# Optimization experiments

Measured on AMD Instinct MI355X. Metric: run time of the kernel, lower is better.

## Reference

```python
import jax, jax.numpy as jnp
import numpy as np

B, S, D = 2, 2048, 2048
H, KV, HD = 16, 4, 128          # n_heads, n_kv_heads, head_dim = d_model // n_heads
R = H // KV                      # n_rep (GQA group size)
THETA = 500000.0


def _rotate_half(x):
    x1, x2 = jnp.split(x, 2, axis=-1)
    return jnp.concatenate([-x2, x1], axis=-1)


def _rope_cos_sin(position_ids):
    # inv_freq over even dims, outer with positions, duplicated (LLaMA-style)
    inv_freq = 1.0 / (THETA ** (jnp.arange(0, HD, 2, dtype=jnp.float32) / HD))
    freqs = position_ids.astype(jnp.float32)[..., None] * inv_freq  # (B, S, HD/2)
    emb = jnp.concatenate([freqs, freqs], axis=-1)                  # (B, S, HD)
    return jnp.cos(emb)[:, None], jnp.sin(emb)[:, None]             # (B, 1, S, HD)


def setup_inputs() -> dict:
    key = jax.random.key(0)
    ks = jax.random.split(key, 5)
    x = jax.random.normal(ks[0], (B, S, D), dtype=jnp.float32)
    wq = jax.random.normal(ks[1], (D, H * HD), dtype=jnp.float32) * (D ** -0.5)
    wk = jax.random.normal(ks[2], (D, KV * HD), dtype=jnp.float32) * (D ** -0.5)
    wv = jax.random.normal(ks[3], (D, KV * HD), dtype=jnp.float32) * (D ** -0.5)
    wo = jax.random.normal(ks[4], (H * HD, D), dtype=jnp.float32) * (D ** -0.5)
    causal = jnp.tril(jnp.ones((S, S), dtype=bool))
    attn_mask = jnp.where(causal, 0.0, -1e9).astype(jnp.float32)[None, None]  # (1,1,S,S)
    position_ids = jnp.tile(jnp.arange(S, dtype=jnp.int32)[None, :], (B, 1))
    return {"x": x, "wq": wq, "wk": wk, "wv": wv, "wo": wo,
            "attn_mask": attn_mask, "position_ids": position_ids}


def reference(x, wq, wk, wv, wo, attn_mask, position_ids):
    b, s, _ = x.shape
    # projections (bias-free Linear) + head split, (B, heads, S, HD)
    q = (x @ wq).reshape(b, s, H, HD).transpose(0, 2, 1, 3)
    k = (x @ wk).reshape(b, s, KV, HD).transpose(0, 2, 1, 3)
    v = (x @ wv).reshape(b, s, KV, HD).transpose(0, 2, 1, 3)
    cos, sin = _rope_cos_sin(position_ids)
    q = q * cos + _rotate_half(q) * sin
    k = k * cos + _rotate_half(k) * sin
    # GQA: group q heads (B, KV, R, S, HD); equivalent to repeat_interleave on K/V
    qg = q.reshape(b, KV, R, s, HD)
    scores = jnp.einsum('bgrsd,bgtd->bgrst', qg.astype(jnp.float32),
                        k.astype(jnp.float32)) / np.float32(np.sqrt(HD))
    scores = scores + attn_mask[:, :, None]          # (1,1,1,S,S) broadcast
    p = jax.nn.softmax(scores, axis=-1).astype(x.dtype)
    out = jnp.einsum('bgrst,bgtd->bgrsd', p, v)      # (B, KV, R, S, HD)
    out = out.reshape(b, H, s, HD).transpose(0, 2, 1, 3).reshape(b, s, H * HD)
    return out @ wo
```

## Files before the change

### kernel.cpp

```cpp
#include <hip/hip_runtime.h>
#include <hip/hip_bf16.h>
#include <math.h>

#define Bsz 2
#define Sq  2048
#define Dm  2048
#define Hn  16
#define KVn 4
#define HDn 128

typedef __attribute__((ext_vector_type(8))) short bf16x8;
typedef __attribute__((ext_vector_type(4))) float f32x4;

__device__ __forceinline__ short f2b(float f) {
    __hip_bfloat16 h = __float2bfloat16(f);
    return *reinterpret_cast<short*>(&h);
}
__device__ __forceinline__ float b2f(short s) {
    __hip_bfloat16 h = *reinterpret_cast<__hip_bfloat16*>(&s);
    return __bfloat162float(h);
}

__global__ __launch_bounds__(256) void f2b_kernel(
    const float* __restrict__ X, short* __restrict__ Y, int n4)
{
    int i = blockIdx.x * 256 + threadIdx.x;
    if (i >= n4) return;
    float4 v = ((const float4*)X)[i];
    short4 o;
    o.x = f2b(v.x); o.y = f2b(v.y); o.z = f2b(v.z); o.w = f2b(v.w);
    ((short4*)Y)[i] = o;
}

__global__ __launch_bounds__(256) void wconv_all_kernel(
    const float* __restrict__ wq, const float* __restrict__ wk,
    const float* __restrict__ wv, const float* __restrict__ wo,
    short* __restrict__ wqkvT, short* __restrict__ woT)
{
    __shared__ float t[32][33];
    const int n0 = blockIdx.x * 32;
    const int k0 = blockIdx.y * 32;
    const int tx = threadIdx.x, ty = threadIdx.y;

    const float* W; int Nsec, nloc; short* dst;
    if (n0 < 2048)      { W = wq; Nsec = 2048; nloc = n0;        dst = wqkvT + (size_t)n0 * Dm; }
    else if (n0 < 2560) { W = wk; Nsec = 512;  nloc = n0 - 2048; dst = wqkvT + (size_t)n0 * Dm; }
    else if (n0 < 3072) { W = wv; Nsec = 512;  nloc = n0 - 2560; dst = wqkvT + (size_t)n0 * Dm; }
    else                { W = wo; Nsec = 2048; nloc = n0 - 3072; dst = woT + (size_t)(n0 - 3072) * Dm; }

#pragma unroll
    for (int r = 0; r < 4; ++r) {
        const int row = ty + 8 * r;
        t[row][tx] = W[(size_t)(k0 + row) * Nsec + nloc + tx];
    }
    __syncthreads();
#pragma unroll
    for (int r = 0; r < 4; ++r) {
        const int row = ty + 8 * r;
        dst[(size_t)row * Dm + k0 + tx] = f2b(t[tx][row]);
    }
}

template <typename OT>
__global__ __launch_bounds__(256) void gemm_bt_kernel(
    const short* __restrict__ A, const short* __restrict__ Bt,
    OT* __restrict__ C, int M, int N, int K)
{
    __shared__ __align__(16) short As[128 * 64];
    __shared__ __align__(16) short Bs[128 * 64];

    const int tid  = threadIdx.x;
    const int w    = tid >> 6;
    const int lane = tid & 63;
    const int m16  = lane & 15;
    const int g4   = lane >> 4;
    const int wm   = w >> 1, wn = w & 1;

    const int row0 = blockIdx.y * 128;
    const int col0 = blockIdx.x * 128;

    const short* Ab = A  + (size_t)row0 * K;
    const short* Bb = Bt + (size_t)col0 * K;

    const int trow = tid >> 3;
    const int soct = (tid & 7) ^ (trow & 7);

    f32x4 acc[4][4];
#pragma unroll
    for (int i = 0; i < 4; ++i)
#pragma unroll
        for (int j = 0; j < 4; ++j) acc[i][j] = (f32x4){0.f, 0.f, 0.f, 0.f};

    for (int k0 = 0; k0 < K; k0 += 64) {
#pragma unroll
        for (int r = 0; r < 4; ++r) {
            const short* gp = Ab + (size_t)(r * 32 + trow) * K + k0 + soct * 8;
            short* lp = &As[(size_t)(r * 256 + w * 64) * 8];
            __builtin_amdgcn_global_load_lds(
                (const __attribute__((address_space(1))) void*)gp,
                (__attribute__((address_space(3))) void*)lp, 16, 0, 0);
        }
#pragma unroll
        for (int r = 0; r < 4; ++r) {
            const short* gp = Bb + (size_t)(r * 32 + trow) * K + k0 + soct * 8;
            short* lp = &Bs[(size_t)(r * 256 + w * 64) * 8];
            __builtin_amdgcn_global_load_lds(
                (const __attribute__((address_space(1))) void*)gp,
                (__attribute__((address_space(3))) void*)lp, 16, 0, 0);
        }
        __syncthreads();

#pragma unroll
        for (int kc = 0; kc < 2; ++kc) {
            bf16x8 a[4], b[4];
            const int swz = (kc * 4 + g4) ^ (m16 & 7);
#pragma unroll
            for (int s = 0; s < 4; ++s) {
                const int rowA = wm * 64 + s * 16 + m16;
                a[s] = *(const bf16x8*)&As[rowA * 64 + swz * 8];
                const int rowB = wn * 64 + s * 16 + m16;
                b[s] = *(const bf16x8*)&Bs[rowB * 64 + swz * 8];
            }
#pragma unroll
            for (int i = 0; i < 4; ++i)
#pragma unroll
                for (int j = 0; j < 4; ++j)
                    acc[i][j] = __builtin_amdgcn_mfma_f32_16x16x32_bf16(
                        a[i], b[j], acc[i][j], 0, 0, 0);
        }
        __syncthreads();
    }

#pragma unroll
    for (int i = 0; i < 4; ++i) {
        const int mbase = row0 + wm * 64 + i * 16 + g4 * 4;
#pragma unroll
        for (int j = 0; j < 4; ++j) {
            const int n = col0 + wn * 64 + j * 16 + m16;
#pragma unroll
            for (int r = 0; r < 4; ++r) {
                if constexpr (sizeof(OT) == 2)
                    C[(size_t)(mbase + r) * N + n] = f2b(acc[i][j][r]);
                else
                    C[(size_t)(mbase + r) * N + n] = acc[i][j][r];
            }
        }
    }
}

__global__ __launch_bounds__(256) void rope_all_kernel(
    const short* __restrict__ C3b, short* __restrict__ Qb, short* __restrict__ Kb,
    const int* __restrict__ pos_ids, float qscale, int total)
{
    int idx = blockIdx.x * blockDim.x + threadIdx.x;
    if (idx >= total) return;
    const int i = idx & 63;
    int rest = idx >> 6;
    const int s = rest % Sq;
    const int b = rest / Sq;

    const int pos = pos_ids[b * Sq + s];
    const float e   = -(float)(2 * i) * (1.0f / (float)HDn);
    const float inv = exp2f(e * 18.931568569324174f);
    const float f   = (float)pos * inv;
    float sn, c;
    sincosf(f, &sn, &c);

    const short* src = C3b + ((size_t)(b * Sq + s)) * 3072;

#pragma unroll
    for (int h = 0; h < Hn; ++h) {
        const float x1 = b2f(src[h * HDn + i]);
        const float x2 = b2f(src[h * HDn + i + 64]);
        const size_t dst = (((size_t)b * Hn + h) * Sq + s) * HDn;
        Qb[dst + i]      = f2b((x1 * c - x2 * sn) * qscale);
        Qb[dst + i + 64] = f2b((x2 * c + x1 * sn) * qscale);
    }
#pragma unroll
    for (int h = 0; h < KVn; ++h) {
        const float x1 = b2f(src[2048 + h * HDn + i]);
        const float x2 = b2f(src[2048 + h * HDn + i + 64]);
        const size_t dst = (((size_t)b * KVn + h) * Sq + s) * HDn;
        Kb[dst + i]      = f2b(x1 * c - x2 * sn);
        Kb[dst + i + 64] = f2b(x2 * c + x1 * sn);
    }
}

__global__ __launch_bounds__(256) void vconv_kernel(
    const short* __restrict__ C3b, short* __restrict__ Vt)
{
    __shared__ short t[32][34];
    const int bk = blockIdx.z;
    const int b  = bk >> 2, kv = bk & 3;
    const int s0 = blockIdx.x * 32;
    const int d0 = blockIdx.y * 32;
    const int tx = threadIdx.x, ty = threadIdx.y;

#pragma unroll
    for (int r = 0; r < 4; ++r) {
        const int row = ty + 8 * r;
        t[row][tx] = C3b[((size_t)(b * Sq + s0 + row)) * 3072 + 2560 + kv * HDn + d0 + tx];
    }
    __syncthreads();
#pragma unroll
    for (int r = 0; r < 4; ++r) {
        const int row = ty + 8 * r;
        Vt[((size_t)bk * HDn + d0 + row) * Sq + s0 + tx] = t[tx][row];
    }
}

__global__ __launch_bounds__(256, 2) void fattn_kernel(
    const short* __restrict__ Qb, const short* __restrict__ Kb,
    const short* __restrict__ Vtb, short* __restrict__ AOb)
{
    __shared__ __align__(16) short Ks[2][64 * 128];
    __shared__ __align__(16) short Vs[2][128 * 64];

    const int tid  = threadIdx.x;
    const int w    = tid >> 6;
    const int lane = tid & 63;
    const int m16  = lane & 15;
    const int g4   = lane >> 4;

    const int i    = blockIdx.x;
    const int half = i >> 8;
    const int k4   = i & 15;
    const int qt   = half ? k4 : 15 - k4;
    const int bh   = i >> 4;
    const int h    = bh & 15;
    const int b    = bh >> 4;
    const int kv   = h >> 2;
    const int q0   = qt << 7;
    const int qA   = q0 + w * 16;
    const int qB   = q0 + 64 + w * 16;

    bf16x8 qf[2][4];
#pragma unroll
    for (int j = 0; j < 2; ++j) {
        const short* qp = Qb + (((size_t)b * Hn + h) * Sq + (j ? qB : qA) + m16) * HDn + g4 * 8;
#pragma unroll
        for (int c = 0; c < 4; ++c) qf[j][c] = *(const bf16x8*)(qp + c * 32);
    }

    const short* kbase = Kb  + ((size_t)b * KVn + kv) * Sq * HDn;
    const short* vbase = Vtb + ((size_t)b * KVn + kv) * (size_t)HDn * Sq;

    const short* gpK[4];
    const short* gpV[4];
#pragma unroll
    for (int r = 0; r < 4; ++r) {
        const int ci = r * 256 + tid;
        const int R  = ci >> 4, o = ci & 15;
        const int hf = (R >> 5) & 1, Rl = R & 31;
        const int phys = hf * 32 + ((Rl >> 2) & 3) * 8 + ((Rl >> 4) & 1) * 4 + (Rl & 3);
        gpK[r] = kbase + (size_t)phys * HDn + (o ^ (R & 7)) * 8;
        const int d = ci >> 3, ov = ci & 7;
        gpV[r] = vbase + (size_t)d * Sq + (ov ^ (d & 7)) * 8;
    }

    f32x4 Ot[2][8];
#pragma unroll
    for (int j = 0; j < 2; ++j)
#pragma unroll
        for (int t = 0; t < 8; ++t) Ot[j][t] = (f32x4){0.f, 0.f, 0.f, 0.f};
    float mcur[2] = {-1e30f, -1e30f}, lcur[2] = {0.f, 0.f};

    const int nch = qt * 2 + 2;

    auto stage = [&](int ch, int buf) {
        const size_t kt = (size_t)(ch << 6);
#pragma unroll
        for (int r = 0; r < 4; ++r) {
            const short* gp = gpK[r] + kt * HDn;
            short* lp = &Ks[buf][(size_t)(r * 256 + w * 64) * 8];
            __builtin_amdgcn_global_load_lds(
                (const __attribute__((address_space(1))) void*)gp,
                (__attribute__((address_space(3))) void*)lp, 16, 0, 0);
        }
#pragma unroll
        for (int r = 0; r < 4; ++r) {
            const short* gp = gpV[r] + kt;
            short* lp = &Vs[buf][(size_t)(r * 256 + w * 64) * 8];
            __builtin_amdgcn_global_load_lds(
                (const __attribute__((address_space(1))) void*)gp,
                (__attribute__((address_space(3))) void*)lp, 16, 0, 0);
        }
    };

    stage(0, 0);

    for (int ch = 0; ch < nch; ++ch) {
        const int cur = ch & 1;
        const int kt  = ch << 6;

        __syncthreads();
        if (ch + 1 < nch) stage(ch + 1, cur ^ 1);

        const bool last  = (ch == nch - 1);
        const bool diag0 = (ch == nch - 2);

        const short* KsC = Ks[cur];
        const short* VsC = Vs[cur];

        f32x4 sc0[4], sc1[4];
        __builtin_amdgcn_s_setprio(1);
#pragma unroll
        for (int f = 0; f < 4; ++f) {
            f32x4 a0 = (f32x4){0.f, 0.f, 0.f, 0.f};
            f32x4 a1 = (f32x4){0.f, 0.f, 0.f, 0.f};
            const int krow = f * 16 + m16;
#pragma unroll
            for (int c = 0; c < 4; ++c) {
                bf16x8 kf = *(const bf16x8*)&KsC[krow * 128 + (((c * 4 + g4) ^ (m16 & 7)) * 8)];
                a0 = __builtin_amdgcn_mfma_f32_16x16x32_bf16(kf, qf[0][c], a0, 0, 0, 0);
                a1 = __builtin_amdgcn_mfma_f32_16x16x32_bf16(kf, qf[1][c], a1, 0, 0, 0);
            }
            sc0[f] = a0; sc1[f] = a1;
        }
        __builtin_amdgcn_s_setprio(0);

        if (diag0) {
            const int qg = qA + m16;
#pragma unroll
            for (int f = 0; f < 4; ++f)
#pragma unroll
                for (int ii = 0; ii < 4; ++ii) {
                    const int kg = kt + (f >> 1) * 32 + g4 * 8 + (f & 1) * 4 + ii;
                    if (kg > qg) sc0[f][ii] = -1e30f;
                }
        }
        if (last) {
            const int qg = qB + m16;
#pragma unroll
            for (int f = 0; f < 4; ++f)
#pragma unroll
                for (int ii = 0; ii < 4; ++ii) {
                    const int kg = kt + (f >> 1) * 32 + g4 * 8 + (f & 1) * 4 + ii;
                    if (kg > qg) sc1[f][ii] = -1e30f;
                }
        }

        bf16x8 pf0[2], pf1[2];
        if (!last) {
            float mx = sc0[0][0];
#pragma unroll
            for (int f = 0; f < 4; ++f)
#pragma unroll
                for (int ii = 0; ii < 4; ++ii) mx = fmaxf(mx, sc0[f][ii]);
            mx = fmaxf(mx, __shfl_xor(mx, 16));
            mx = fmaxf(mx, __shfl_xor(mx, 32));
            if (!__all(mx <= mcur[0] + 8.0f)) {
                const float nm = fmaxf(mcur[0], mx);
                const float alpha = exp2f(mcur[0] - nm);
                mcur[0] = nm;
                lcur[0] *= alpha;
#pragma unroll
                for (int t = 0; t < 8; ++t)
#pragma unroll
                    for (int ii = 0; ii < 4; ++ii) Ot[0][t][ii] *= alpha;
            }
            float ps = 0.f;
#pragma unroll
            for (int f = 0; f < 4; ++f)
#pragma unroll
                for (int ii = 0; ii < 4; ++ii) {
                    sc0[f][ii] = exp2f(sc0[f][ii] - mcur[0]);
                    ps += sc0[f][ii];
                }
            ps += __shfl_xor(ps, 16);
            ps += __shfl_xor(ps, 32);
            lcur[0] += ps;
#pragma unroll
            for (int hf = 0; hf < 2; ++hf) {
                bf16x8 p;
#pragma unroll
                for (int j8 = 0; j8 < 8; ++j8)
                    p[j8] = f2b(j8 < 4 ? sc0[hf * 2][j8] : sc0[hf * 2 + 1][j8 - 4]);
                pf0[hf] = p;
            }
        }
        {
            float mx = sc1[0][0];
#pragma unroll
            for (int f = 0; f < 4; ++f)
#pragma unroll
                for (int ii = 0; ii < 4; ++ii) mx = fmaxf(mx, sc1[f][ii]);
            mx = fmaxf(mx, __shfl_xor(mx, 16));
            mx = fmaxf(mx, __shfl_xor(mx, 32));
            if (!__all(mx <= mcur[1] + 8.0f)) {
                const float nm = fmaxf(mcur[1], mx);
                const float alpha = exp2f(mcur[1] - nm);
                mcur[1] = nm;
                lcur[1] *= alpha;
#pragma unroll
                for (int t = 0; t < 8; ++t)
#pragma unroll
                    for (int ii = 0; ii < 4; ++ii) Ot[1][t][ii] *= alpha;
            }
            float ps = 0.f;
#pragma unroll
            for (int f = 0; f < 4; ++f)
#pragma unroll
                for (int ii = 0; ii < 4; ++ii) {
                    sc1[f][ii] = exp2f(sc1[f][ii] - mcur[1]);
                    ps += sc1[f][ii];
                }
            ps += __shfl_xor(ps, 16);
            ps += __shfl_xor(ps, 32);
            lcur[1] += ps;
#pragma unroll
            for (int hf = 0; hf < 2; ++hf) {
                bf16x8 p;
#pragma unroll
                for (int j8 = 0; j8 < 8; ++j8)
                    p[j8] = f2b(j8 < 4 ? sc1[hf * 2][j8] : sc1[hf * 2 + 1][j8 - 4]);
                pf1[hf] = p;
            }
        }

        __builtin_amdgcn_s_setprio(1);
#pragma unroll
        for (int t = 0; t < 8; ++t) {
            const int d = t * 16 + m16;
            bf16x8 vfa = *(const bf16x8*)&VsC[d * 64 + ((g4 ^ (d & 7)) * 8)];
            bf16x8 vfb = *(const bf16x8*)&VsC[d * 64 + (((4 + g4) ^ (d & 7)) * 8)];
            if (!last) {
                Ot[0][t] = __builtin_amdgcn_mfma_f32_16x16x32_bf16(vfa, pf0[0], Ot[0][t], 0, 0, 0);
                Ot[0][t] = __builtin_amdgcn_mfma_f32_16x16x32_bf16(vfb, pf0[1], Ot[0][t], 0, 0, 0);
            }
            Ot[1][t] = __builtin_amdgcn_mfma_f32_16x16x32_bf16(vfa, pf1[0], Ot[1][t], 0, 0, 0);
            Ot[1][t] = __builtin_amdgcn_mfma_f32_16x16x32_bf16(vfb, pf1[1], Ot[1][t], 0, 0, 0);
        }
        __builtin_amdgcn_s_setprio(0);
    }

#pragma unroll
    for (int j = 0; j < 2; ++j) {
        const float inv = 1.0f / lcur[j];
        short* op = AOb + ((size_t)b * Sq + (j ? qB : qA) + m16) * (Hn * HDn) + h * HDn + g4 * 4;
#pragma unroll
        for (int t = 0; t < 8; ++t) {
            short4 o;
            o.x = f2b(Ot[j][t][0] * inv);
            o.y = f2b(Ot[j][t][1] * inv);
            o.z = f2b(Ot[j][t][2] * inv);
            o.w = f2b(Ot[j][t][3] * inv);
            *(short4*)(op + t * 16) = o;
        }
    }
}

extern "C" void kernel_launch(void* const* d_in, const int* in_sizes, int n_in,
                              void* d_out, int out_size, void* d_ws, size_t ws_size,
                              hipStream_t stream)
{
    const float* x   = (const float*)d_in[0];
    const float* wq  = (const float*)d_in[1];
    const float* wk  = (const float*)d_in[2];
    const float* wv  = (const float*)d_in[3];
    const float* wo  = (const float*)d_in[4];
    const int* pos   = (const int*)d_in[6];
    float* out = (float*)d_out;

    const int M = Bsz * Sq;
    const size_t nX  = (size_t)M * Dm;

    short* xb    = (short*)d_ws;
    short* wqkvT = xb + nX;
    short* woT   = wqkvT + (size_t)3072 * Dm;
    short* C3b   = woT + (size_t)Dm * Dm;
    short* Qb    = C3b + (size_t)M * 3072;
    short* Kb    = Qb + nX;
    short* Vtb   = Kb + (size_t)Bsz * KVn * Sq * HDn;
    short* AOb   = Vtb + (size_t)Bsz * KVn * Sq * HDn;

    f2b_kernel<<<(nX / 4 + 255) / 256, 256, 0, stream>>>(x, xb, nX / 4);
    wconv_all_kernel<<<dim3(5120 / 32, Dm / 32), dim3(32, 8), 0, stream>>>(
        wq, wk, wv, wo, wqkvT, woT);

    gemm_bt_kernel<short><<<dim3(3072 / 128, M / 128), 256, 0, stream>>>(
        xb, wqkvT, C3b, M, 3072, Dm);

    {
        const float qscale = 0.08838834764831845f * 1.4426950408889634f;
        int tot = Bsz * Sq * 64;
        rope_all_kernel<<<(tot + 255) / 256, 256, 0, stream>>>(
            C3b, Qb, Kb, pos, qscale, tot);
    }
    vconv_kernel<<<dim3(Sq / 32, HDn / 32, Bsz * KVn), dim3(32, 8), 0, stream>>>(
        C3b, Vtb);

    fattn_kernel<<<Bsz * Hn * (Sq / 128), 256, 0, stream>>>(Qb, Kb, Vtb, AOb);

    gemm_bt_kernel<float><<<dim3(Dm / 128, M / 128), 256, 0, stream>>>(
        AOb, woT, out, M, Dm, Dm);
}
```

Baseline: 330.0 us.

## Pair complementary 64-row query tiles per block for causal load balance

```diff
diff --git a/kernel.cpp b/kernel.cpp
--- a/kernel.cpp
+++ b/kernel.cpp
@@ -222,24 +222,24 @@
     const int m16  = lane & 15;
     const int g4   = lane >> 4;
 
-    const int i    = blockIdx.x;
-    const int half = i >> 8;
-    const int k4   = i & 15;
-    const int qt   = half ? k4 : 15 - k4;
-    const int bh   = i >> 4;
-    const int h    = bh & 15;
-    const int b    = bh >> 4;
-    const int kv   = h >> 2;
-    const int q0   = qt << 7;
-    const int qA   = q0 + w * 16;
-    const int qB   = q0 + 64 + w * 16;
-
-    bf16x8 qf[2][4];
-#pragma unroll
-    for (int j = 0; j < 2; ++j) {
-        const short* qp = Qb + (((size_t)b * Hn + h) * Sq + (j ? qB : qA) + m16) * HDn + g4 * 8;
-#pragma unroll
-        for (int c = 0; c < 4; ++c) qf[j][c] = *(const bf16x8*)(qp + c * 32);
+    const int p  = blockIdx.x & 15;
+    const int h  = (blockIdx.x >> 4) & 15;
+    const int b  = blockIdx.x >> 8;
+    const int kv = h >> 2;
+
+    const int htA = 31 - p, htB = p;
+    const int nchA = htA + 1, nchB = htB + 1;
+    const int qbA = htA << 6, qbB = htB << 6;
+
+    bf16x8 qfA[4], qfB[4];
+    {
+        const short* qpA = Qb + (((size_t)b * Hn + h) * Sq + qbA + w * 16 + m16) * HDn + g4 * 8;
+        const short* qpB = Qb + (((size_t)b * Hn + h) * Sq + qbB + w * 16 + m16) * HDn + g4 * 8;
+#pragma unroll
+        for (int c = 0; c < 4; ++c) {
+            qfA[c] = *(const bf16x8*)(qpA + c * 32);
+            qfB[c] = *(const bf16x8*)(qpB + c * 32);
+        }
     }
 
     const short* kbase = Kb  + ((size_t)b * KVn + kv) * Sq * HDn;
@@ -258,20 +258,10 @@
         gpV[r] = vbase + (size_t)d * Sq + (ov ^ (d & 7)) * 8;
     }
 
-    f32x4 Ot[2][8];
-#pragma unroll
-    for (int j = 0; j < 2; ++j)
-#pragma unroll
-        for (int t = 0; t < 8; ++t) Ot[j][t] = (f32x4){0.f, 0.f, 0.f, 0.f};
-    float mcur[2] = {-1e30f, -1e30f}, lcur[2] = {0.f, 0.f};
-
-    const int nch = qt * 2 + 2;
-
-    auto stage = [&](int ch, int buf) {
-        const size_t kt = (size_t)(ch << 6);
+    auto stage = [&](int ktE, int buf) {
 #pragma unroll
         for (int r = 0; r < 4; ++r) {
-            const short* gp = gpK[r] + kt * HDn;
+            const short* gp = gpK[r] + (size_t)ktE * HDn;
             short* lp = &Ks[buf][(size_t)(r * 256 + w * 64) * 8];
             __builtin_amdgcn_global_load_lds(
                 (const __attribute__((address_space(1))) void*)gp,
@@ -279,7 +269,7 @@
         }
 #pragma unroll
         for (int r = 0; r < 4; ++r) {
-            const short* gp = gpV[r] + kt;
+            const short* gp = gpV[r] + ktE;
             short* lp = &Vs[buf][(size_t)(r * 256 + w * 64) * 8];
             __builtin_amdgcn_global_load_lds(
                 (const __attribute__((address_space(1))) void*)gp,
@@ -287,167 +277,126 @@
         }
     };
 
-    stage(0, 0);
-
-    for (int ch = 0; ch < nch; ++ch) {
-        const int cur = ch & 1;
-        const int kt  = ch << 6;
-
-        __syncthreads();
-        if (ch + 1 < nch) stage(ch + 1, cur ^ 1);
-
-        const bool last  = (ch == nch - 1);
-        const bool diag0 = (ch == nch - 2);
-
-        const short* KsC = Ks[cur];
-        const short* VsC = Vs[cur];
-
-        f32x4 sc0[4], sc1[4];
-        __builtin_amdgcn_s_setprio(1);
-#pragma unroll
-        for (int f = 0; f < 4; ++f) {
-            f32x4 a0 = (f32x4){0.f, 0.f, 0.f, 0.f};
-            f32x4 a1 = (f32x4){0.f, 0.f, 0.f, 0.f};
-            const int krow = f * 16 + m16;
-#pragma unroll
-            for (int c = 0; c < 4; ++c) {
-                bf16x8 kf = *(const bf16x8*)&KsC[krow * 128 + (((c * 4 + g4) ^ (m16 & 7)) * 8)];
-                a0 = __builtin_amdgcn_mfma_f32_16x16x32_bf16(kf, qf[0][c], a0, 0, 0, 0);
-                a1 = __builtin_amdgcn_mfma_f32_16x16x32_bf16(kf, qf[1][c], a1, 0, 0, 0);
-            }
-            sc0[f] = a0; sc1[f] = a1;
-        }
-        __builtin_amdgcn_s_setprio(0);
-
-        if (diag0) {
-            const int qg = qA + m16;
+    f32x4 Ot[8];
+#pragma unroll
+    for (int t = 0; t < 8; ++t) Ot[t] = (f32x4){0.f, 0.f, 0.f, 0.f};
+    float mcur = -1e30f, lcur = 0.f;
+    int gpar = 0;
+
+    auto run_job = [&](const bf16x8 (&qf)[4], int nch, int qb, bool lastJob) {
+        for (int ch = 0; ch < nch; ++ch) {
+            const int cur = gpar & 1;
+            gpar ^= 1;
+            const int kt = ch << 6;
+
+            __syncthreads();
+            if (ch + 1 < nch)      stage((ch + 1) << 6, cur ^ 1);
+            else if (!lastJob)     stage(0, cur ^ 1);
+
+            const bool diag = (ch == nch - 1);
+            const short* KsC = Ks[cur];
+            const short* VsC = Vs[cur];
+
+            f32x4 sc[4];
+            __builtin_amdgcn_s_setprio(1);
+#pragma unroll
+            for (int f = 0; f < 4; ++f) {
+                f32x4 a = (f32x4){0.f, 0.f, 0.f, 0.f};
+                const int krow = f * 16 + m16;
+#pragma unroll
+                for (int c = 0; c < 4; ++c) {
+                    bf16x8 kf = *(const bf16x8*)&KsC[krow * 128 + (((c * 4 + g4) ^ (m16 & 7)) * 8)];
+                    a = __builtin_amdgcn_mfma_f32_16x16x32_bf16(kf, qf[c], a, 0, 0, 0);
+                }
+                sc[f] = a;
+            }
+            __builtin_amdgcn_s_setprio(0);
+
+            if (diag) {
+                const int qg = qb + w * 16 + m16;
+#pragma unroll
+                for (int f = 0; f < 4; ++f)
+#pragma unroll
+                    for (int ii = 0; ii < 4; ++ii) {
+                        const int kg = kt + (f >> 1) * 32 + g4 * 8 + (f & 1) * 4 + ii;
+                        if (kg > qg) sc[f][ii] = -1e30f;
+                    }
+            }
+
+            float mx = sc[0][0];
 #pragma unroll
             for (int f = 0; f < 4; ++f)
 #pragma unroll
-                for (int ii = 0; ii < 4; ++ii) {
-                    const int kg = kt + (f >> 1) * 32 + g4 * 8 + (f & 1) * 4 + ii;
-                    if (kg > qg) sc0[f][ii] = -1e30f;
-                }
-        }
-        if (last) {
-            const int qg = qB + m16;
-#pragma unroll
-            for (int f = 0; f < 4; ++f)
-#pragma unroll
-                for (int ii = 0; ii < 4; ++ii) {
-                    const int kg = kt + (f >> 1) * 32 + g4 * 8 + (f & 1) * 4 + ii;
-                    if (kg > qg) sc1[f][ii] = -1e30f;
-                }
-        }
-
-        bf16x8 pf0[2], pf1[2];
-        if (!last) {
-            float mx = sc0[0][0];
-#pragma unroll
-            for (int f = 0; f < 4; ++f)
-#pragma unroll
-                for (int ii = 0; ii < 4; ++ii) mx = fmaxf(mx, sc0[f][ii]);
+                for (int ii = 0; ii < 4; ++ii) mx = fmaxf(mx, sc[f][ii]);
             mx = fmaxf(mx, __shfl_xor(mx, 16));
             mx = fmaxf(mx, __shfl_xor(mx, 32));
-            if (!__all(mx <= mcur[0] + 8.0f)) {
-                const float nm = fmaxf(mcur[0], mx);
-                const float alpha = exp2f(mcur[0] - nm);
-                mcur[0] = nm;
-                lcur[0] *= alpha;
+            if (!__all(mx <= mcur + 8.0f)) {
+                const float nm = fmaxf(mcur, mx);
+                const float alpha = exp2f(mcur - nm);
+                mcur = nm;
+                lcur *= alpha;
 #pragma unroll
                 for (int t = 0; t < 8; ++t)
 #pragma unroll
-                    for (int ii = 0; ii < 4; ++ii) Ot[0][t][ii] *= alpha;
+                    for (int ii = 0; ii < 4; ++ii) Ot[t][ii] *= alpha;
             }
             float ps = 0.f;
 #pragma unroll
             for (int f = 0; f < 4; ++f)
 #pragma unroll
                 for (int ii = 0; ii < 4; ++ii) {
-                    sc0[f][ii] = exp2f(sc0[f][ii] - mcur[0]);
-                    ps += sc0[f][ii];
+                    sc[f][ii] = exp2f(sc[f][ii] - mcur);
+                    ps += sc[f][ii];
                 }
             ps += __shfl_xor(ps, 16);
             ps += __shfl_xor(ps, 32);
-            lcur[0] += ps;
+            lcur += ps;
+
+            bf16x8 pf[2];
 #pragma unroll
             for (int hf = 0; hf < 2; ++hf) {
-                bf16x8 p;
+                bf16x8 pk;
 #pragma unroll
                 for (int j8 = 0; j8 < 8; ++j8)
-                    p[j8] = f2b(j8 < 4 ? sc0[hf * 2][j8] : sc0[hf * 2 + 1][j8 - 4]);
-                pf0[hf] = p;
-            }
-        }
-        {
-            float mx = sc1[0][0];
-#pragma unroll
-            for (int f = 0; f < 4; ++f)
-#pragma unroll
-                for (int ii = 0; ii < 4; ++ii) mx = fmaxf(mx, sc1[f][ii]);
-            mx = fmaxf(mx, __shfl_xor(mx, 16));
-            mx = fmaxf(mx, __shfl_xor(mx, 32));
-            if (!__all(mx <= mcur[1] + 8.0f)) {
-                const float nm = fmaxf(mcur[1], mx);
-                const float alpha = exp2f(mcur[1] - nm);
-                mcur[1] = nm;
-                lcur[1] *= alpha;
-#pragma unroll
-                for (int t = 0; t < 8; ++t)
-#pragma unroll
-                    for (int ii = 0; ii < 4; ++ii) Ot[1][t][ii] *= alpha;
-            }
-            float ps = 0.f;
-#pragma unroll
-            for (int f = 0; f < 4; ++f)
-#pragma unroll
-                for (int ii = 0; ii < 4; ++ii) {
-                    sc1[f][ii] = exp2f(sc1[f][ii] - mcur[1]);
-                    ps += sc1[f][ii];
-                }
-            ps += __shfl_xor(ps, 16);
-            ps += __shfl_xor(ps, 32);
-            lcur[1] += ps;
-#pragma unroll
-            for (int hf = 0; hf < 2; ++hf) {
-                bf16x8 p;
-#pragma unroll
-                for (int j8 = 0; j8 < 8; ++j8)
-                    p[j8] = f2b(j8 < 4 ? sc1[hf * 2][j8] : sc1[hf * 2 + 1][j8 - 4]);
-                pf1[hf] = p;
-            }
-        }
-
-        __builtin_amdgcn_s_setprio(1);
-#pragma unroll
-        for (int t = 0; t < 8; ++t) {
-            const int d = t * 16 + m16;
-            bf16x8 vfa = *(const bf16x8*)&VsC[d * 64 + ((g4 ^ (d & 7)) * 8)];
-            bf16x8 vfb = *(const bf16x8*)&VsC[d * 64 + (((4 + g4) ^ (d & 7)) * 8)];
-            if (!last) {
-                Ot[0][t] = __builtin_amdgcn_mfma_f32_16x16x32_bf16(vfa, pf0[0], Ot[0][t], 0, 0, 0);
-                Ot[0][t] = __builtin_amdgcn_mfma_f32_16x16x32_bf16(vfb, pf0[1], Ot[0][t], 0, 0, 0);
-            }
-            Ot[1][t] = __builtin_amdgcn_mfma_f32_16x16x32_bf16(vfa, pf1[0], Ot[1][t], 0, 0, 0);
-            Ot[1][t] = __builtin_amdgcn_mfma_f32_16x16x32_bf16(vfb, pf1[1], Ot[1][t], 0, 0, 0);
-        }
-        __builtin_amdgcn_s_setprio(0);
-    }
-
-#pragma unroll
-    for (int j = 0; j < 2; ++j) {
-        const float inv = 1.0f / lcur[j];
-        short* op = AOb + ((size_t)b * Sq + (j ? qB : qA) + m16) * (Hn * HDn) + h * HDn + g4 * 4;
+                    pk[j8] = f2b(j8 < 4 ? sc[hf * 2][j8] : sc[hf * 2 + 1][j8 - 4]);
+                pf[hf] = pk;
+            }
+
+            __builtin_amdgcn_s_setprio(1);
+#pragma unroll
+            for (int t = 0; t < 8; ++t) {
+                const int d = t * 16 + m16;
+                bf16x8 vfa = *(const bf16x8*)&VsC[d * 64 + ((g4 ^ (d & 7)) * 8)];
+                bf16x8 vfb = *(const bf16x8*)&VsC[d * 64 + (((4 + g4) ^ (d & 7)) * 8)];
+                Ot[t] = __builtin_amdgcn_mfma_f32_16x16x32_bf16(vfa, pf[0], Ot[t], 0, 0, 0);
+                Ot[t] = __builtin_amdgcn_mfma_f32_16x16x32_bf16(vfb, pf[1], Ot[t], 0, 0, 0);
+            }
+            __builtin_amdgcn_s_setprio(0);
+        }
+    };
+
+    auto writeO = [&](int qb) {
+        const float inv = 1.0f / lcur;
+        short* op = AOb + ((size_t)(b * Sq + qb + w * 16 + m16)) * (Hn * HDn) + h * HDn + g4 * 4;
 #pragma unroll
         for (int t = 0; t < 8; ++t) {
             short4 o;
-            o.x = f2b(Ot[j][t][0] * inv);
-            o.y = f2b(Ot[j][t][1] * inv);
-            o.z = f2b(Ot[j][t][2] * inv);
-            o.w = f2b(Ot[j][t][3] * inv);
+            o.x = f2b(Ot[t][0] * inv);
+            o.y = f2b(Ot[t][1] * inv);
+            o.z = f2b(Ot[t][2] * inv);
+            o.w = f2b(Ot[t][3] * inv);
             *(short4*)(op + t * 16) = o;
         }
-    }
+    };
+
+    stage(0, 0);
+    run_job(qfA, nchA, qbA, false);
+    writeO(qbA);
+#pragma unroll
+    for (int t = 0; t < 8; ++t) Ot[t] = (f32x4){0.f, 0.f, 0.f, 0.f};
+    mcur = -1e30f; lcur = 0.f;
+    run_job(qfB, nchB, qbB, true);
+    writeO(qbB);
 }
 
 extern "C" void kernel_launch(void* const* d_in, const int* in_sizes, int n_in,
```

Measured after the change: 323.8 us. No clear change (-1.9%).

## Pair mirrored 64-row query tiles per block to balance causal attention work

Applied to the files above, without the earlier changes.

```diff
diff --git a/kernel.cpp b/kernel.cpp
--- a/kernel.cpp
+++ b/kernel.cpp
@@ -225,21 +225,25 @@
     const int i    = blockIdx.x;
     const int half = i >> 8;
     const int k4   = i & 15;
-    const int qt   = half ? k4 : 15 - k4;
-    const int bh   = i >> 4;
-    const int h    = bh & 15;
-    const int b    = bh >> 4;
+    const int p    = half ? k4 : 15 - k4;
+    const int h    = (i >> 4) & 15;
+    const int b    = i >> 8;
     const int kv   = h >> 2;
-    const int q0   = qt << 7;
-    const int qA   = q0 + w * 16;
-    const int qB   = q0 + 64 + w * 16;
-
-    bf16x8 qf[2][4];
-#pragma unroll
-    for (int j = 0; j < 2; ++j) {
-        const short* qp = Qb + (((size_t)b * Hn + h) * Sq + (j ? qB : qA) + m16) * HDn + g4 * 8;
-#pragma unroll
-        for (int c = 0; c < 4; ++c) qf[j][c] = *(const bf16x8*)(qp + c * 32);
+
+    const int htA = 31 - p, htB = p;
+    const int nch = htA + 1;
+    const int qA  = htA * 64 + w * 16;
+    const int qB  = htB * 64 + w * 16;
+
+    bf16x8 qfA[4], qfB[4];
+    {
+        const short* qpA = Qb + (((size_t)b * Hn + h) * Sq + qA + m16) * HDn + g4 * 8;
+        const short* qpB = Qb + (((size_t)b * Hn + h) * Sq + qB + m16) * HDn + g4 * 8;
+#pragma unroll
+        for (int c = 0; c < 4; ++c) {
+            qfA[c] = *(const bf16x8*)(qpA + c * 32);
+            qfB[c] = *(const bf16x8*)(qpB + c * 32);
+        }
     }
 
     const short* kbase = Kb  + ((size_t)b * KVn + kv) * Sq * HDn;
@@ -258,20 +262,10 @@
         gpV[r] = vbase + (size_t)d * Sq + (ov ^ (d & 7)) * 8;
     }
 
-    f32x4 Ot[2][8];
-#pragma unroll
-    for (int j = 0; j < 2; ++j)
-#pragma unroll
-        for (int t = 0; t < 8; ++t) Ot[j][t] = (f32x4){0.f, 0.f, 0.f, 0.f};
-    float mcur[2] = {-1e30f, -1e30f}, lcur[2] = {0.f, 0.f};
-
-    const int nch = qt * 2 + 2;
-
-    auto stage = [&](int ch, int buf) {
-        const size_t kt = (size_t)(ch << 6);
+    auto stage = [&](int ktE, int buf) {
 #pragma unroll
         for (int r = 0; r < 4; ++r) {
-            const short* gp = gpK[r] + kt * HDn;
+            const short* gp = gpK[r] + (size_t)ktE * HDn;
             short* lp = &Ks[buf][(size_t)(r * 256 + w * 64) * 8];
             __builtin_amdgcn_global_load_lds(
                 (const __attribute__((address_space(1))) void*)gp,
@@ -279,7 +273,7 @@
         }
 #pragma unroll
         for (int r = 0; r < 4; ++r) {
-            const short* gp = gpV[r] + kt;
+            const short* gp = gpV[r] + ktE;
             short* lp = &Vs[buf][(size_t)(r * 256 + w * 64) * 8];
             __builtin_amdgcn_global_load_lds(
                 (const __attribute__((address_space(1))) void*)gp,
@@ -287,18 +281,25 @@
         }
     };
 
+    f32x4 OtA[8], OtB[8];
+#pragma unroll
+    for (int t = 0; t < 8; ++t) {
+        OtA[t] = (f32x4){0.f, 0.f, 0.f, 0.f};
+        OtB[t] = (f32x4){0.f, 0.f, 0.f, 0.f};
+    }
+    float mA = -1e30f, lA = 0.f, mB = -1e30f, lB = 0.f;
+
     stage(0, 0);
-
-    for (int ch = 0; ch < nch; ++ch) {
-        const int cur = ch & 1;
+    int gpar = 0;
+
+    for (int ch = 0; ch <= p; ++ch) {
+        const int cur = gpar & 1; gpar ^= 1;
         const int kt  = ch << 6;
 
         __syncthreads();
-        if (ch + 1 < nch) stage(ch + 1, cur ^ 1);
-
-        const bool last  = (ch == nch - 1);
-        const bool diag0 = (ch == nch - 2);
-
+        stage((ch + 1) << 6, cur ^ 1);
+
+        const bool dgB = (ch == p);
         const short* KsC = Ks[cur];
         const short* VsC = Vs[cur];
 
@@ -312,24 +313,14 @@
 #pragma unroll
             for (int c = 0; c < 4; ++c) {
                 bf16x8 kf = *(const bf16x8*)&KsC[krow * 128 + (((c * 4 + g4) ^ (m16 & 7)) * 8)];
-                a0 = __builtin_amdgcn_mfma_f32_16x16x32_bf16(kf, qf[0][c], a0, 0, 0, 0);
-                a1 = __builtin_amdgcn_mfma_f32_16x16x32_bf16(kf, qf[1][c], a1, 0, 0, 0);
+                a0 = __builtin_amdgcn_mfma_f32_16x16x32_bf16(kf, qfA[c], a0, 0, 0, 0);
+                a1 = __builtin_amdgcn_mfma_f32_16x16x32_bf16(kf, qfB[c], a1, 0, 0, 0);
             }
             sc0[f] = a0; sc1[f] = a1;
         }
         __builtin_amdgcn_s_setprio(0);
 
-        if (diag0) {
-            const int qg = qA + m16;
-#pragma unroll
-            for (int f = 0; f < 4; ++f)
-#pragma unroll
-                for (int ii = 0; ii < 4; ++ii) {
-                    const int kg = kt + (f >> 1) * 32 + g4 * 8 + (f & 1) * 4 + ii;
-                    if (kg > qg) sc0[f][ii] = -1e30f;
-                }
-        }
-        if (last) {
+        if (dgB) {
             const int qg = qB + m16;
 #pragma unroll
             for (int f = 0; f < 4; ++f)
@@ -341,7 +332,7 @@
         }
 
         bf16x8 pf0[2], pf1[2];
-        if (!last) {
+        {
             float mx = sc0[0][0];
 #pragma unroll
             for (int f = 0; f < 4; ++f)
@@ -349,34 +340,33 @@
                 for (int ii = 0; ii < 4; ++ii) mx = fmaxf(mx, sc0[f][ii]);
             mx = fmaxf(mx, __shfl_xor(mx, 16));
             mx = fmaxf(mx, __shfl_xor(mx, 32));
-            if (!__all(mx <= mcur[0] + 8.0f)) {
-                const float nm = fmaxf(mcur[0], mx);
-                const float alpha = exp2f(mcur[0] - nm);
-                mcur[0] = nm;
-                lcur[0] *= alpha;
+            if (!__all(mx <= mA + 8.0f)) {
+                const float nm = fmaxf(mA, mx);
+                const float alpha = exp2f(mA - nm);
+                mA = nm; lA *= alpha;
 #pragma unroll
                 for (int t = 0; t < 8; ++t)
 #pragma unroll
-                    for (int ii = 0; ii < 4; ++ii) Ot[0][t][ii] *= alpha;
+                    for (int ii = 0; ii < 4; ++ii) OtA[t][ii] *= alpha;
             }
             float ps = 0.f;
 #pragma unroll
             for (int f = 0; f < 4; ++f)
 #pragma unroll
                 for (int ii = 0; ii < 4; ++ii) {
-                    sc0[f][ii] = exp2f(sc0[f][ii] - mcur[0]);
+                    sc0[f][ii] = exp2f(sc0[f][ii] - mA);
                     ps += sc0[f][ii];
                 }
             ps += __shfl_xor(ps, 16);
             ps += __shfl_xor(ps, 32);
-            lcur[0] += ps;
+            lA += ps;
 #pragma unroll
             for (int hf = 0; hf < 2; ++hf) {
-                bf16x8 p;
+                bf16x8 pk;
 #pragma unroll
                 for (int j8 = 0; j8 < 8; ++j8)
-                    p[j8] = f2b(j8 < 4 ? sc0[hf * 2][j8] : sc0[hf * 2 + 1][j8 - 4]);
-                pf0[hf] = p;
+                    pk[j8] = f2b(j8 < 4 ? sc0[hf * 2][j8] : sc0[hf * 2 + 1][j8 - 4]);
+                pf0[hf] = pk;
             }
         }
         {
@@ -387,34 +377,33 @@
                 for (int ii = 0; ii < 4; ++ii) mx = fmaxf(mx, sc1[f][ii]);
             mx = fmaxf(mx, __shfl_xor(mx, 16));
             mx = fmaxf(mx, __shfl_xor(mx, 32));
-            if (!__all(mx <= mcur[1] + 8.0f)) {
-                const float nm = fmaxf(mcur[1], mx);
-                const float alpha = exp2f(mcur[1] - nm);
-                mcur[1] = nm;
-                lcur[1] *= alpha;
+            if (!__all(mx <= mB + 8.0f)) {
+                const float nm = fmaxf(mB, mx);
+                const float alpha = exp2f(mB - nm);
+                mB = nm; lB *= alpha;
 #pragma unroll
                 for (int t = 0; t < 8; ++t)
 #pragma unroll
-                    for (int ii = 0; ii < 4; ++ii) Ot[1][t][ii] *= alpha;
+                    for (int ii = 0; ii < 4; ++ii) OtB[t][ii] *= alpha;
             }
             float ps = 0.f;
 #pragma unroll
             for (int f = 0; f < 4; ++f)
 #pragma unroll
                 for (int ii = 0; ii < 4; ++ii) {
-                    sc1[f][ii] = exp2f(sc1[f][ii] - mcur[1]);
+                    sc1[f][ii] = exp2f(sc1[f][ii] - mB);
                     ps += sc1[f][ii];
                 }
             ps += __shfl_xor(ps, 16);
             ps += __shfl_xor(ps, 32);
-            lcur[1] += ps;
+            lB += ps;
 #pragma unroll
             for (int hf = 0; hf < 2; ++hf) {
-                bf16x8 p;
+                bf16x8 pk;
 #pragma unroll
                 for (int j8 = 0; j8 < 8; ++j8)
-                    p[j8] = f2b(j8 < 4 ? sc1[hf * 2][j8] : sc1[hf * 2 + 1][j8 - 4]);
-                pf1[hf] = p;
+                    pk[j8] = f2b(j8 < 4 ? sc1[hf * 2][j8] : sc1[hf * 2 + 1][j8 - 4]);
+                pf1[hf] = pk;
             }
         }
 
@@ -424,27 +413,125 @@
             const int d = t * 16 + m16;
             bf16x8 vfa = *(const bf16x8*)&VsC[d * 64 + ((g4 ^ (d & 7)) * 8)];
             bf16x8 vfb = *(const bf16x8*)&VsC[d * 64 + (((4 + g4) ^ (d & 7)) * 8)];
-            if (!last) {
-                Ot[0][t] = __builtin_amdgcn_mfma_f32_16x16x32_bf16(vfa, pf0[0], Ot[0][t], 0, 0, 0);
-                Ot[0][t] = __builtin_amdgcn_mfma_f32_16x16x32_bf16(vfb, pf0[1], Ot[0][t], 0, 0, 0);
-            }
-            Ot[1][t] = __builtin_amdgcn_mfma_f32_16x16x32_bf16(vfa, pf1[0], Ot[1][t], 0, 0, 0);
-            Ot[1][t] = __builtin_amdgcn_mfma_f32_16x16x32_bf16(vfb, pf1[1], Ot[1][t], 0, 0, 0);
+            OtA[t] = __builtin_amdgcn_mfma_f32_16x16x32_bf16(vfa, pf0[0], OtA[t], 0, 0, 0);
+            OtA[t] = __builtin_amdgcn_mfma_f32_16x16x32_bf16(vfb, pf0[1], OtA[t], 0, 0, 0);
+            OtB[t] = __builtin_amdgcn_mfma_f32_16x16x32_bf16(vfa, pf1[0], OtB[t], 0, 0, 0);
+            OtB[t] = __builtin_amdgcn_mfma_f32_16x16x32_bf16(vfb, pf1[1], OtB[t], 0, 0, 0);
         }
         __builtin_amdgcn_s_setprio(0);
     }
 
-#pragma unroll
-    for (int j = 0; j < 2; ++j) {
-        const float inv = 1.0f / lcur[j];
-        short* op = AOb + ((size_t)b * Sq + (j ? qB : qA) + m16) * (Hn * HDn) + h * HDn + g4 * 4;
+    {
+        const float inv = 1.0f / lB;
+        short* op = AOb + ((size_t)(b * Sq + qB + m16)) * (Hn * HDn) + h * HDn + g4 * 4;
 #pragma unroll
         for (int t = 0; t < 8; ++t) {
             short4 o;
-            o.x = f2b(Ot[j][t][0] * inv);
-            o.y = f2b(Ot[j][t][1] * inv);
-            o.z = f2b(Ot[j][t][2] * inv);
-            o.w = f2b(Ot[j][t][3] * inv);
+            o.x = f2b(OtB[t][0] * inv);
+            o.y = f2b(OtB[t][1] * inv);
+            o.z = f2b(OtB[t][2] * inv);
+            o.w = f2b(OtB[t][3] * inv);
+            *(short4*)(op + t * 16) = o;
+        }
+    }
+
+    for (int ch = p + 1; ch < nch; ++ch) {
+        const int cur = gpar & 1; gpar ^= 1;
+        const int kt  = ch << 6;
+
+        __syncthreads();
+        if (ch + 1 < nch) stage((ch + 1) << 6, cur ^ 1);
+
+        const bool dgA = (ch == nch - 1);
+        const short* KsC = Ks[cur];
+        const short* VsC = Vs[cur];
+
+        f32x4 sc[4];
+        __builtin_amdgcn_s_setprio(1);
+#pragma unroll
+        for (int f = 0; f < 4; ++f) {
+            f32x4 a = (f32x4){0.f, 0.f, 0.f, 0.f};
+            const int krow = f * 16 + m16;
+#pragma unroll
+            for (int c = 0; c < 4; ++c) {
+                bf16x8 kf = *(const bf16x8*)&KsC[krow * 128 + (((c * 4 + g4) ^ (m16 & 7)) * 8)];
+                a = __builtin_amdgcn_mfma_f32_16x16x32_bf16(kf, qfA[c], a, 0, 0, 0);
+            }
+            sc[f] = a;
+        }
+        __builtin_amdgcn_s_setprio(0);
+
+        if (dgA) {
+            const int qg = qA + m16;
+#pragma unroll
+            for (int f = 0; f < 4; ++f)
+#pragma unroll
+                for (int ii = 0; ii < 4; ++ii) {
+                    const int kg = kt + (f >> 1) * 32 + g4 * 8 + (f & 1) * 4 + ii;
+                    if (kg > qg) sc[f][ii] = -1e30f;
+                }
+        }
+
+        float mx = sc[0][0];
+#pragma unroll
+        for (int f = 0; f < 4; ++f)
+#pragma unroll
+            for (int ii = 0; ii < 4; ++ii) mx = fmaxf(mx, sc[f][ii]);
+        mx = fmaxf(mx, __shfl_xor(mx, 16));
+        mx = fmaxf(mx, __shfl_xor(mx, 32));
+        if (!__all(mx <= mA + 8.0f)) {
+            const float nm = fmaxf(mA, mx);
+            const float alpha = exp2f(mA - nm);
+            mA = nm; lA *= alpha;
+#pragma unroll
+            for (int t = 0; t < 8; ++t)
+#pragma unroll
+                for (int ii = 0; ii < 4; ++ii) OtA[t][ii] *= alpha;
+        }
+        float ps = 0.f;
+#pragma unroll
+        for (int f = 0; f < 4; ++f)
+#pragma unroll
+            for (int ii = 0; ii < 4; ++ii) {
+                sc[f][ii] = exp2f(sc[f][ii] - mA);
+                ps += sc[f][ii];
+            }
+        ps += __shfl_xor(ps, 16);
+        ps += __shfl_xor(ps, 32);
+        lA += ps;
+
+        bf16x8 pf[2];
+#pragma unroll
+        for (int hf = 0; hf < 2; ++hf) {
+            bf16x8 pk;
+#pragma unroll
+            for (int j8 = 0; j8 < 8; ++j8)
+                pk[j8] = f2b(j8 < 4 ? sc[hf * 2][j8] : sc[hf * 2 + 1][j8 - 4]);
+            pf[hf] = pk;
+        }
+
+        __builtin_amdgcn_s_setprio(1);
+#pragma unroll
+        for (int t = 0; t < 8; ++t) {
+            const int d = t * 16 + m16;
+            bf16x8 vfa = *(const bf16x8*)&VsC[d * 64 + ((g4 ^ (d & 7)) * 8)];
+            bf16x8 vfb = *(const bf16x8*)&VsC[d * 64 + (((4 + g4) ^ (d & 7)) * 8)];
+            OtA[t] = __builtin_amdgcn_mfma_f32_16x16x32_bf16(vfa, pf[0], OtA[t], 0, 0, 0);
+            OtA[t] = __builtin_amdgcn_mfma_f32_16x16x32_bf16(vfb, pf[1], OtA[t], 0, 0, 0);
+        }
+        __builtin_amdgcn_s_setprio(0);
+    }
+
+    {
+        const float inv = 1.0f / lA;
+        short* op = AOb + ((size_t)(b * Sq + qA + m16)) * (Hn * HDn) + h * HDn + g4 * 4;
+#pragma unroll
+        for (int t = 0; t < 8; ++t) {
+            short4 o;
+            o.x = f2b(OtA[t][0] * inv);
+            o.y = f2b(OtA[t][1] * inv);
+            o.z = f2b(OtA[t][2] * inv);
+            o.w = f2b(OtA[t][3] * inv);
             *(short4*)(op + t * 16) = o;
         }
     }
@@ -490,7 +577,7 @@
     vconv_kernel<<<dim3(Sq / 32, HDn / 32, Bsz * KVn), dim3(32, 8), 0, stream>>>(
         C3b, Vtb);
 
-    fattn_kernel<<<Bsz * Hn * (Sq / 128), 256, 0, stream>>>(Qb, Kb, Vtb, AOb);
+    fattn_kernel<<<Bsz * Hn * 16, 256, 0, stream>>>(Qb, Kb, Vtb, AOb);
 
     gemm_bt_kernel<float><<<dim3(Dm / 128, M / 128), 256, 0, stream>>>(
         AOb, woT, out, M, Dm, Dm);
```

New measurement: 315.4 us. 4.4% less time.
